# Optimization experiments

Measured on AMD Instinct MI355X. Metric: run time of the kernel, lower is better.

## Reference

```python
import jax, jax.numpy as jnp
import numpy as np

N_NODES = 50000


def gin_conv(x, src, dst, W, b, eps=0.0):
    # GINConv: nn((1+eps)*x_i + sum_{j in N(i)} x_j)
    agg = jax.ops.segment_sum(x[src], dst, num_segments=N_NODES)  # [N, D]
    h = (1.0 + eps) * x + agg
    return h @ W + b


def setup_inputs() -> dict:
    key = jax.random.key(0)
    ks = jax.random.split(key, 8)
    n, e = N_NODES, 800000
    d_in, d_h, d_out = 128, 128, 64
    feature = jax.random.normal(ks[0], (n, d_in), dtype=jnp.float32)
    edge_index = jax.random.randint(ks[1], (2, e), 0, n, dtype=jnp.int64)
    s1 = 1.0 / np.sqrt(d_in)
    sh = 1.0 / np.sqrt(d_h)
    W1 = jax.random.normal(ks[2], (d_in, d_h), dtype=jnp.float32) * s1
    b1 = jnp.zeros((d_h,), dtype=jnp.float32)
    Wh = jax.random.normal(ks[3], (d_h, d_h), dtype=jnp.float32) * sh
    bh = jnp.zeros((d_h,), dtype=jnp.float32)
    Wo = jax.random.normal(ks[4], (d_h, d_out), dtype=jnp.float32) * sh
    bo = jnp.zeros((d_out,), dtype=jnp.float32)
    return {"feature": feature, "edge_index": edge_index, "W1": W1, "b1": b1,
            "Wh": Wh, "bh": bh, "Wo": Wo, "bo": bo}


def reference(feature, edge_index, W1, b1, Wh, bh, Wo, bo):
    src, dst = edge_index[0], edge_index[1]
    x = gin_conv(feature, src, dst, W1, b1)
    x = jax.nn.relu(x)
    # one hidden layer (layer_num=3); dropout disabled (eval)
    x = gin_conv(x, src, dst, Wh, bh)
    x = jax.nn.relu(x)
    x = gin_conv(x, src, dst, Wo, bo)
    return jax.nn.log_softmax(x, axis=1)
```

## Files before the change

### kernel.cpp

```cpp
#include <hip/hip_runtime.h>

typedef short short8 __attribute__((ext_vector_type(8)));
typedef float f32x4 __attribute__((ext_vector_type(4)));


__device__ inline unsigned short f2bf(float f) {
    union { float f; unsigned u; } v; v.f = f;
    unsigned r = v.u + 0x7fffu + ((v.u >> 16) & 1u);
    return (unsigned short)(r >> 16);
}
__device__ inline unsigned pack2(float a, float b) {
    return (unsigned)f2bf(a) | ((unsigned)f2bf(b) << 16);
}
__device__ inline float bflo(unsigned u) { union { unsigned q; float f; } c; c.q = u << 16; return c.f; }
__device__ inline float bfhi(unsigned u) { union { unsigned q; float f; } c; c.q = u & 0xffff0000u; return c.f; }

#define ACC8(vv)                                     \
    acc[0] += bflo(vv.x); acc[1] += bfhi(vv.x);      \
    acc[2] += bflo(vv.y); acc[3] += bfhi(vv.y);      \
    acc[4] += bflo(vv.z); acc[5] += bfhi(vv.z);      \
    acc[6] += bflo(vv.w); acc[7] += bfhi(vv.w);

template <int TPN, typename F>
__device__ __forceinline__ void gather_acc(float acc[8], const uint4* __restrict__ x,
                                           int lane, int beg, int end, F geti) {
    int k = beg;
    for (; k + 8 <= end; k += 8) {
        int idx[8];
#pragma unroll
        for (int j = 0; j < 8; j++) idx[j] = geti(k + j);
        uint4 v[8];
#pragma unroll
        for (int j = 0; j < 8; j++) v[j] = x[(size_t)idx[j] * TPN + lane];
#pragma unroll
        for (int j = 0; j < 8; j++) { ACC8(v[j]) }
    }
    for (; k + 4 <= end; k += 4) {
        int i0 = geti(k), i1 = geti(k + 1), i2 = geti(k + 2), i3 = geti(k + 3);
        uint4 v0 = x[(size_t)i0 * TPN + lane];
        uint4 v1 = x[(size_t)i1 * TPN + lane];
        uint4 v2 = x[(size_t)i2 * TPN + lane];
        uint4 v3 = x[(size_t)i3 * TPN + lane];
        ACC8(v0) ACC8(v1) ACC8(v2) ACC8(v3)
    }
    for (; k < end; ++k) {
        uint4 v0 = x[(size_t)geti(k) * TPN + lane];
        ACC8(v0)
    }
}


#define EPB 2048
#define NE 8
#define BSH 9
#define MAXBKT 128
#define DCAP 10240
#define BCAP 16384

__global__ __launch_bounds__(256) void megaA(
    const int* __restrict__ src, const int* __restrict__ dst,
    int* __restrict__ cursor, unsigned* __restrict__ pairs,
    int e, int nbkt, int nblk,
    const float4* __restrict__ feat, uint2* __restrict__ featb, int cvtb, int nf4,
    const float* __restrict__ W1, const float* __restrict__ Wh, const float* __restrict__ Wo,
    unsigned short* __restrict__ W1t, unsigned short* __restrict__ Wht,
    unsigned short* __restrict__ Wot) {
    __shared__ int hist[MAXBKT], loff[MAXBKT], cur[MAXBKT], gb[MAXBKT];
    __shared__ int sc[256];
    __shared__ unsigned sorted[EPB];
    int t = threadIdx.x, blk = blockIdx.x;
    if (blk < nblk) {
        for (int b = t; b < nbkt; b += 256) hist[b] = 0;
        __syncthreads();
        int base = blk * EPB;
        int cnt = min(EPB, e - base);
        unsigned packed[NE];
        int bb[NE];
#pragma unroll
        for (int j = 0; j < NE; j++) {
            int idx = base + t + 256 * j;
            bb[j] = -1;
            if (idx < e) {
                unsigned s0 = (unsigned)src[idx], d = (unsigned)dst[idx];
                int b = (int)(d >> BSH);
                bb[j] = b;
                packed[j] = s0 | ((d & ((1u << BSH) - 1)) << 16) | ((unsigned)b << 25);
                atomicAdd(&hist[b], 1);
            }
        }
        __syncthreads();
        int v = (t < nbkt) ? hist[t] : 0;
        sc[t] = v;
        __syncthreads();
        for (int off = 1; off < 256; off <<= 1) {
            int u = (t >= off) ? sc[t - off] : 0;
            __syncthreads();
            sc[t] += u;
            __syncthreads();
        }
        if (t < nbkt) {
            int ex = sc[t] - v;
            loff[t] = ex;
            cur[t] = ex;
            gb[t] = t * BCAP + (v ? atomicAdd(&cursor[t], v) : atomicAdd(&cursor[t], 0));
        }
        __syncthreads();
#pragma unroll
        for (int j = 0; j < NE; j++) {
            if (bb[j] >= 0) {
                int r = atomicAdd(&cur[bb[j]], 1);
                sorted[r] = packed[j];
            }
        }
        __syncthreads();
        for (int i = t; i < cnt; i += 256) {
            unsigned w = sorted[i];
            int b = (int)(w >> 25);
            pairs[gb[b] + (i - loff[b])] = w;
        }
    } else if (blk < nblk + cvtb) {
        int i = (blk - nblk) * 256 + t;
        if (i < nf4) {
            float4 v = feat[i];
            featb[i] = make_uint2(pack2(v.x, v.y), pack2(v.z, v.w));
        }
    } else {
        int i = (blk - nblk - cvtb) * 256 + t;
        if (i < 16384) {
            int k = i >> 7, nn = i & 127;
            W1t[nn * 128 + k] = f2bf(W1[i]);
        } else if (i < 32768) {
            int j = i - 16384, k = j >> 7, nn = j & 127;
            Wht[nn * 128 + k] = f2bf(Wh[j]);
        } else if (i < 40960) {
            int j = i - 32768, k = j >> 6, nn = j & 63;
            Wot[nn * 128 + k] = f2bf(Wo[j]);
        }
    }
}

__global__ __launch_bounds__(512) void buildD(const unsigned* __restrict__ pairs,
                                              const int* __restrict__ cursor,
                                              int* __restrict__ row_ptr, int* __restrict__ row_end,
                                              unsigned short* __restrict__ csr, int n) {
    __shared__ int hist[512], off[512];
    __shared__ unsigned short lcsr[DCAP];
    int t = threadIdx.x, b = blockIdx.x;
    int cnt = cursor[b], base = b * BCAP;
    hist[t] = 0;
    __syncthreads();
    for (int i = t; i < cnt; i += 512)
        atomicAdd(&hist[(pairs[base + i] >> 16) & 511], 1);
    __syncthreads();
    int v = hist[t];
    off[t] = v;
    __syncthreads();
    for (int o = 1; o < 512; o <<= 1) {
        int u = (t >= o) ? off[t - o] : 0;
        __syncthreads();
        off[t] += u;
        __syncthreads();
    }
    int excl = off[t] - v;
    int node = (b << BSH) + t;
    if (node < n) {
        row_ptr[node] = base + excl;
        row_end[node] = base + off[t];
    }
    __syncthreads();
    hist[t] = excl;
    __syncthreads();
    for (int i = t; i < cnt; i += 512) {
        unsigned w = pairs[base + i];
        int r = atomicAdd(&hist[(w >> 16) & 511], 1);
        if (r < DCAP) lcsr[r] = (unsigned short)(w & 0xFFFFu);
    }
    __syncthreads();
    int lim = min(cnt, DCAP);
    for (int i = t; i < lim; i += 512) csr[base + i] = lcsr[i];
}


#define ECAP 1024

template <bool SECOND>
__global__ __launch_bounds__(256) void fused_layer(
    const uint4* __restrict__ x, const int* __restrict__ row_ptr,
    const int* __restrict__ row_end, const unsigned short* __restrict__ csr,
    const short8* __restrict__ Bt, const float* __restrict__ bias,
    unsigned short* __restrict__ out_h,
    const short8* __restrict__ Bt2,
    unsigned short* __restrict__ out_y,
    int n) {
    __shared__ unsigned short As[16][136];
    __shared__ unsigned short Hs[SECOND ? 16 : 1][SECOND ? 136 : 1];
    __shared__ unsigned short eidx[ECAP];

    int t = threadIdx.x;
    int nl = t >> 4, chunk = t & 15;
    int r0 = blockIdx.x * 16;
    int node = r0 + nl;

    int E0 = row_ptr[min(r0, n - 1)];
    int E1 = row_end[min(r0 + 15, n - 1)];
    int ecnt = min(E1 - E0, ECAP);
    for (int i = t; i < ecnt; i += 256) eidx[i] = csr[E0 + i];
    __syncthreads();

    float acc[8] = {0.f, 0.f, 0.f, 0.f, 0.f, 0.f, 0.f, 0.f};
    if (node < n) {
        uint4 s0 = x[(size_t)node * 16 + chunk];
        ACC8(s0)
        int beg = row_ptr[node], end = row_end[node];
        if (E1 - E0 <= ECAP) {
            gather_acc<16>(acc, x, chunk, beg - E0, end - E0,
                           [&](int k) { return (int)eidx[k]; });
        } else {
            gather_acc<16>(acc, x, chunk, beg, end,
                           [&](int k) { return (int)csr[k]; });
        }
    }
    uint4 packed;
    packed.x = pack2(acc[0], acc[1]); packed.y = pack2(acc[2], acc[3]);
    packed.z = pack2(acc[4], acc[5]); packed.w = pack2(acc[6], acc[7]);
    ((uint4*)&As[nl][0])[chunk] = packed;
    __syncthreads();

    int wid = t >> 6, lane = t & 63;
    int lm = lane & 15, lq = lane >> 4;

    short8 a[4];
#pragma unroll
    for (int kc = 0; kc < 4; kc++)
        a[kc] = *(const short8*)&As[lm][kc * 32 + lq * 8];

    f32x4 hacc[2];
#pragma unroll
    for (int nt = 0; nt < 2; nt++) hacc[nt] = (f32x4){0.f, 0.f, 0.f, 0.f};
#pragma unroll
    for (int nt = 0; nt < 2; nt++) {
        const short8* Br = Bt + (size_t)((wid * 2 + nt) * 16 + lm) * 16;
#pragma unroll
        for (int kc = 0; kc < 4; kc++)
            hacc[nt] = __builtin_amdgcn_mfma_f32_16x16x32_bf16(a[kc], Br[kc * 4 + lq], hacc[nt], 0, 0, 0);
    }

#pragma unroll
    for (int nt = 0; nt < 2; nt++) {
        int col = (wid * 2 + nt) * 16 + lm;
        float bv = bias[col];
#pragma unroll
        for (int i = 0; i < 4; i++) {
            int row = r0 + lq * 4 + i;
            float v = fmaxf(hacc[nt][i] + bv, 0.f);
            if (SECOND) {
                Hs[lq * 4 + i][col] = f2bf(v);
            } else if (row < n) {
                out_h[(size_t)row * 128 + col] = f2bf(v);
            }
        }
    }

    if (SECOND) {
        __syncthreads();
        short8 a2[4];
#pragma unroll
        for (int kc = 0; kc < 4; kc++)
            a2[kc] = *(const short8*)&Hs[lm][kc * 32 + lq * 8];
        f32x4 yacc = (f32x4){0.f, 0.f, 0.f, 0.f};
        const short8* Br2 = Bt2 + (size_t)(wid * 16 + lm) * 16;
#pragma unroll
        for (int kc = 0; kc < 4; kc++)
            yacc = __builtin_amdgcn_mfma_f32_16x16x32_bf16(a2[kc], Br2[kc * 4 + lq], yacc, 0, 0, 0);
        int col = wid * 16 + lm;
#pragma unroll
        for (int i = 0; i < 4; i++) {
            int row = r0 + lq * 4 + i;
            if (row < n) out_y[(size_t)row * 64 + col] = f2bf(yacc[i]);
        }
    }
}


#define ECAP2 1536

__global__ __launch_bounds__(256) void agg_lsm(
    const uint4* __restrict__ x, float* __restrict__ out,
    const int* __restrict__ row_ptr, const int* __restrict__ row_end,
    const unsigned short* __restrict__ csr, const float* __restrict__ bo, int n) {
    __shared__ unsigned short eidx[ECAP2];
    int t = threadIdx.x;
    int r0 = blockIdx.x * 32;
    int node = r0 + (t >> 3), lane = t & 7;

    int E0 = row_ptr[min(r0, n - 1)];
    int E1 = row_end[min(r0 + 31, n - 1)];
    int ecnt = min(E1 - E0, ECAP2);
    for (int i = t; i < ecnt; i += 256) eidx[i] = csr[E0 + i];
    __syncthreads();

    if (node >= n) return;
    uint4 s0 = x[(size_t)node * 8 + lane];
    float acc[8] = { bflo(s0.x), bfhi(s0.x), bflo(s0.y), bfhi(s0.y),
                     bflo(s0.z), bfhi(s0.z), bflo(s0.w), bfhi(s0.w) };
    int beg = row_ptr[node], end = row_end[node];
    if (E1 - E0 <= ECAP2) {
        gather_acc<8>(acc, x, lane, beg - E0, end - E0,
                      [&](int k) { return (int)eidx[k]; });
    } else {
        gather_acc<8>(acc, x, lane, beg, end,
                      [&](int k) { return (int)csr[k]; });
    }

    const float4* bo4 = (const float4*)bo;
    float4 bA = bo4[lane * 2], bB = bo4[lane * 2 + 1];
    acc[0] += bA.x; acc[1] += bA.y; acc[2] += bA.z; acc[3] += bA.w;
    acc[4] += bB.x; acc[5] += bB.y; acc[6] += bB.z; acc[7] += bB.w;
    float m = acc[0];
#pragma unroll
    for (int j = 1; j < 8; j++) m = fmaxf(m, acc[j]);
#pragma unroll
    for (int off = 1; off < 8; off <<= 1) m = fmaxf(m, __shfl_xor(m, off, 64));
    float s = 0.f;
#pragma unroll
    for (int j = 0; j < 8; j++) s += __expf(acc[j] - m);
#pragma unroll
    for (int off = 1; off < 8; off <<= 1) s += __shfl_xor(s, off, 64);
    float ls = m + __logf(s);
    float4 o0 = make_float4(acc[0] - ls, acc[1] - ls, acc[2] - ls, acc[3] - ls);
    float4 o1 = make_float4(acc[4] - ls, acc[5] - ls, acc[6] - ls, acc[7] - ls);
    float4* op = (float4*)(out + (size_t)node * 64 + lane * 8);
    op[0] = o0;
    op[1] = o1;
}


extern "C" void kernel_launch(void* const* d_in, const int* in_sizes, int n_in,
                              void* d_out, int out_size, void* d_ws, size_t ws_size,
                              hipStream_t stream) {
    const float* feature = (const float*)d_in[0];
    const int*   edges   = (const int*)d_in[1];
    const float* W1 = (const float*)d_in[2];
    const float* b1 = (const float*)d_in[3];
    const float* Wh = (const float*)d_in[4];
    const float* bh = (const float*)d_in[5];
    const float* Wo = (const float*)d_in[6];
    const float* bo = (const float*)d_in[7];

    int n = in_sizes[0] / 128;
    int e = in_sizes[1] / 2;
    const int* src = edges;
    const int* dst = edges + e;

    int nbkt = (n + 511) >> BSH;
    int nblk = (e + EPB - 1) / EPB;
    int nf4 = n * 32;
    int cvtb = (nf4 + 255) / 256;

    char* ws = (char*)d_ws;
    auto take = [&](size_t bytes) {
        char* p = ws;
        ws += (bytes + 255) & ~(size_t)255;
        return p;
    };
    int* cursor  = (int*)take((size_t)nbkt * 4);
    int* row_ptr = (int*)take((size_t)n * 4);
    int* row_end = (int*)take((size_t)n * 4);
    unsigned* pairs = (unsigned*)take((size_t)nbkt * BCAP * 4);
    unsigned short* csr = (unsigned short*)take((size_t)nbkt * BCAP * 2);
    unsigned short* featb = (unsigned short*)take((size_t)n * 128 * 2);
    unsigned short* hb    = (unsigned short*)take((size_t)n * 128 * 2);
    unsigned short* yb    = (unsigned short*)take((size_t)n * 64 * 2);
    unsigned short* W1t = (unsigned short*)take(128 * 128 * 2);
    unsigned short* Wht = (unsigned short*)take(128 * 128 * 2);
    unsigned short* Wot = (unsigned short*)take(64 * 128 * 2);

    hipMemsetAsync(cursor, 0, (size_t)nbkt * 4, stream);
    megaA<<<nblk + cvtb + 160, 256, 0, stream>>>(
        src, dst, cursor, pairs, e, nbkt, nblk,
        (const float4*)feature, (uint2*)featb, cvtb, nf4,
        W1, Wh, Wo, W1t, Wht, Wot);
    buildD<<<nbkt, 512, 0, stream>>>(pairs, cursor, row_ptr, row_end, csr, n);

    int fblocks = (n + 15) / 16;

    fused_layer<false><<<fblocks, 256, 0, stream>>>(
        (const uint4*)featb, row_ptr, row_end, csr, (const short8*)W1t, b1,
        hb, nullptr, nullptr, n);

    fused_layer<true><<<fblocks, 256, 0, stream>>>(
        (const uint4*)hb, row_ptr, row_end, csr, (const short8*)Wht, bh,
        nullptr, (const short8*)Wot, yb, n);

    agg_lsm<<<(n + 31) / 32, 256, 0, stream>>>(
        (const uint4*)yb, (float*)d_out, row_ptr, row_end, csr, bo, n);
}
```

Measured before the change: 209.6 us.

## Split each node's edge gather across lane groups with shuffle reduction

The gather/aggregate loops in the fused layer and final aggregation kernels are restructured so that each wavefront handles a few nodes at a time, with lane groups working on interleaved edges of the same node. Partial sums are then combined through cross-lane xor shuffles. The goal is to reduce load imbalance from uneven node degrees and to expose more independent memory loads per node. In exchange it adds shuffle reductions, a serial loop over nodes per wave, and an extra shared-memory staging buffer in the final kernel. It also changes the fp32 summation order.

Result: slower. 229.6 us (+9.5%).

```diff
diff --git a/kernel.cpp b/kernel.cpp
--- a/kernel.cpp
+++ b/kernel.cpp
@@ -21,31 +21,21 @@
     acc[4] += bflo(vv.z); acc[5] += bfhi(vv.z);      \
     acc[6] += bflo(vv.w); acc[7] += bfhi(vv.w);
 
-template <int TPN, typename F>
-__device__ __forceinline__ void gather_acc(float acc[8], const uint4* __restrict__ x,
-                                           int lane, int beg, int end, F geti) {
-    int k = beg;
-    for (; k + 8 <= end; k += 8) {
-        int idx[8];
-#pragma unroll
-        for (int j = 0; j < 8; j++) idx[j] = geti(k + j);
-        uint4 v[8];
-#pragma unroll
-        for (int j = 0; j < 8; j++) v[j] = x[(size_t)idx[j] * TPN + lane];
-#pragma unroll
-        for (int j = 0; j < 8; j++) { ACC8(v[j]) }
-    }
-    for (; k + 4 <= end; k += 4) {
-        int i0 = geti(k), i1 = geti(k + 1), i2 = geti(k + 2), i3 = geti(k + 3);
-        uint4 v0 = x[(size_t)i0 * TPN + lane];
-        uint4 v1 = x[(size_t)i1 * TPN + lane];
-        uint4 v2 = x[(size_t)i2 * TPN + lane];
-        uint4 v3 = x[(size_t)i3 * TPN + lane];
+template <int TPN, int EW, typename F>
+__device__ __forceinline__ void node_gather(float acc[8], const uint4* __restrict__ x,
+                                            int chunk, int eo, int beg, int end, F geti) {
+    int k = beg + eo;
+    for (; k + 3 * EW < end; k += 4 * EW) {
+        int i0 = geti(k), i1 = geti(k + EW), i2 = geti(k + 2 * EW), i3 = geti(k + 3 * EW);
+        uint4 v0 = x[(size_t)i0 * TPN + chunk];
+        uint4 v1 = x[(size_t)i1 * TPN + chunk];
+        uint4 v2 = x[(size_t)i2 * TPN + chunk];
+        uint4 v3 = x[(size_t)i3 * TPN + chunk];
         ACC8(v0) ACC8(v1) ACC8(v2) ACC8(v3)
     }
-    for (; k < end; ++k) {
-        uint4 v0 = x[(size_t)geti(k) * TPN + lane];
-        ACC8(v0)
+    for (; k < end; k += EW) {
+        uint4 v = x[(size_t)geti(k) * TPN + chunk];
+        ACC8(v)
     }
 }
 
@@ -197,36 +187,50 @@
     __shared__ unsigned short eidx[ECAP];
 
     int t = threadIdx.x;
-    int nl = t >> 4, chunk = t & 15;
     int r0 = blockIdx.x * 16;
-    int node = r0 + nl;
+    int wid = t >> 6, lane = t & 63;
+    int chunk = lane & 15, eo = lane >> 4;
 
     int E0 = row_ptr[min(r0, n - 1)];
     int E1 = row_end[min(r0 + 15, n - 1)];
     int ecnt = min(E1 - E0, ECAP);
+    bool staged = (E1 - E0) <= ECAP;
     for (int i = t; i < ecnt; i += 256) eidx[i] = csr[E0 + i];
     __syncthreads();
 
-    float acc[8] = {0.f, 0.f, 0.f, 0.f, 0.f, 0.f, 0.f, 0.f};
-    if (node < n) {
-        uint4 s0 = x[(size_t)node * 16 + chunk];
-        ACC8(s0)
-        int beg = row_ptr[node], end = row_end[node];
-        if (E1 - E0 <= ECAP) {
-            gather_acc<16>(acc, x, chunk, beg - E0, end - E0,
-                           [&](int k) { return (int)eidx[k]; });
-        } else {
-            gather_acc<16>(acc, x, chunk, beg, end,
-                           [&](int k) { return (int)csr[k]; });
-        }
-    }
-    uint4 packed;
-    packed.x = pack2(acc[0], acc[1]); packed.y = pack2(acc[2], acc[3]);
-    packed.z = pack2(acc[4], acc[5]); packed.w = pack2(acc[6], acc[7]);
-    ((uint4*)&As[nl][0])[chunk] = packed;
-    __syncthreads();
-
-    int wid = t >> 6, lane = t & 63;
+#pragma unroll
+    for (int nd = 0; nd < 4; nd++) {
+        int nl = wid * 4 + nd;
+        int node = r0 + nl;
+        float acc[8] = {0.f, 0.f, 0.f, 0.f, 0.f, 0.f, 0.f, 0.f};
+        if (node < n) {
+            if (eo == 0) {
+                uint4 s0 = x[(size_t)node * 16 + chunk];
+                ACC8(s0)
+            }
+            int beg = row_ptr[node], end = row_end[node];
+            if (staged) {
+                node_gather<16, 4>(acc, x, chunk, eo, beg - E0, end - E0,
+                                   [&](int k) { return (int)eidx[k]; });
+            } else {
+                node_gather<16, 4>(acc, x, chunk, eo, beg, end,
+                                   [&](int k) { return (int)csr[k]; });
+            }
+        }
+#pragma unroll
+        for (int j = 0; j < 8; j++) {
+            acc[j] += __shfl_xor(acc[j], 16, 64);
+            acc[j] += __shfl_xor(acc[j], 32, 64);
+        }
+        if (eo == 0) {
+            uint4 packed;
+            packed.x = pack2(acc[0], acc[1]); packed.y = pack2(acc[2], acc[3]);
+            packed.z = pack2(acc[4], acc[5]); packed.w = pack2(acc[6], acc[7]);
+            ((uint4*)&As[nl][0])[chunk] = packed;
+        }
+    }
+    __syncthreads();
+
     int lm = lane & 15, lq = lane >> 4;
 
     short8 a[4];
@@ -289,31 +293,59 @@
     const int* __restrict__ row_ptr, const int* __restrict__ row_end,
     const unsigned short* __restrict__ csr, const float* __restrict__ bo, int n) {
     __shared__ unsigned short eidx[ECAP2];
+    __shared__ float Zs[32][72];
     int t = threadIdx.x;
     int r0 = blockIdx.x * 32;
-    int node = r0 + (t >> 3), lane = t & 7;
+    int wid = t >> 6, lane = t & 63;
+    int chunk = lane & 7, eo = lane >> 3;
 
     int E0 = row_ptr[min(r0, n - 1)];
     int E1 = row_end[min(r0 + 31, n - 1)];
     int ecnt = min(E1 - E0, ECAP2);
+    bool staged = (E1 - E0) <= ECAP2;
     for (int i = t; i < ecnt; i += 256) eidx[i] = csr[E0 + i];
     __syncthreads();
 
+#pragma unroll
+    for (int nd = 0; nd < 8; nd++) {
+        int nl = wid * 8 + nd;
+        int node = r0 + nl;
+        float acc[8] = {0.f, 0.f, 0.f, 0.f, 0.f, 0.f, 0.f, 0.f};
+        if (node < n) {
+            if (eo == 0) {
+                uint4 s0 = x[(size_t)node * 8 + chunk];
+                ACC8(s0)
+            }
+            int beg = row_ptr[node], end = row_end[node];
+            if (staged) {
+                node_gather<8, 8>(acc, x, chunk, eo, beg - E0, end - E0,
+                                  [&](int k) { return (int)eidx[k]; });
+            } else {
+                node_gather<8, 8>(acc, x, chunk, eo, beg, end,
+                                  [&](int k) { return (int)csr[k]; });
+            }
+        }
+#pragma unroll
+        for (int j = 0; j < 8; j++) {
+            acc[j] += __shfl_xor(acc[j], 8, 64);
+            acc[j] += __shfl_xor(acc[j], 16, 64);
+            acc[j] += __shfl_xor(acc[j], 32, 64);
+        }
+        if (eo == 0) {
+#pragma unroll
+            for (int j = 0; j < 8; j++) Zs[nl][chunk * 8 + j] = acc[j];
+        }
+    }
+    __syncthreads();
+
+    int nl = t >> 3, col = t & 7;
+    int node = r0 + nl;
     if (node >= n) return;
-    uint4 s0 = x[(size_t)node * 8 + lane];
-    float acc[8] = { bflo(s0.x), bfhi(s0.x), bflo(s0.y), bfhi(s0.y),
-                     bflo(s0.z), bfhi(s0.z), bflo(s0.w), bfhi(s0.w) };
-    int beg = row_ptr[node], end = row_end[node];
-    if (E1 - E0 <= ECAP2) {
-        gather_acc<8>(acc, x, lane, beg - E0, end - E0,
-                      [&](int k) { return (int)eidx[k]; });
-    } else {
-        gather_acc<8>(acc, x, lane, beg, end,
-                      [&](int k) { return (int)csr[k]; });
-    }
-
+    float acc[8];
+#pragma unroll
+    for (int j = 0; j < 8; j++) acc[j] = Zs[nl][col * 8 + j];
     const float4* bo4 = (const float4*)bo;
-    float4 bA = bo4[lane * 2], bB = bo4[lane * 2 + 1];
+    float4 bA = bo4[col * 2], bB = bo4[col * 2 + 1];
     acc[0] += bA.x; acc[1] += bA.y; acc[2] += bA.z; acc[3] += bA.w;
     acc[4] += bB.x; acc[5] += bB.y; acc[6] += bB.z; acc[7] += bB.w;
     float m = acc[0];
@@ -329,7 +361,7 @@
     float ls = m + __logf(s);
     float4 o0 = make_float4(acc[0] - ls, acc[1] - ls, acc[2] - ls, acc[3] - ls);
     float4 o1 = make_float4(acc[4] - ls, acc[5] - ls, acc[6] - ls, acc[7] - ls);
-    float4* op = (float4*)(out + (size_t)node * 64 + lane * 8);
+    float4* op = (float4*)(out + (size_t)node * 64 + col * 8);
     op[0] = o0;
     op[1] = o1;
 }
```

## Split aggregation and GEMM into separate kernels with column-plane feature layout

Applied to the files above, without the earlier changes.

Features are now stored in 32-column planes, and aggregation runs per plane with four edge slots per node combined by shuffles. This is meant to shrink the gather working set per block so it stays in cache and to raise parallelism. The dense transforms become standalone MFMA GEMM kernels, and the final log-softmax gets its own kernel reading an fp32 intermediate. The cost is extra launches plus writing and re-reading the aggregated and fp32 intermediates through global memory, where the fused version kept them in shared memory.

After: 257.3 us. 1.23x slower.

```diff
diff --git a/kernel.cpp b/kernel.cpp
--- a/kernel.cpp
+++ b/kernel.cpp
@@ -2,6 +2,7 @@
 
 typedef short short8 __attribute__((ext_vector_type(8)));
 typedef float f32x4 __attribute__((ext_vector_type(4)));
+typedef unsigned u32x4 __attribute__((ext_vector_type(4)));
 
 
 __device__ inline unsigned short f2bf(float f) {
@@ -20,34 +21,6 @@
     acc[2] += bflo(vv.y); acc[3] += bfhi(vv.y);      \
     acc[4] += bflo(vv.z); acc[5] += bfhi(vv.z);      \
     acc[6] += bflo(vv.w); acc[7] += bfhi(vv.w);
-
-template <int TPN, typename F>
-__device__ __forceinline__ void gather_acc(float acc[8], const uint4* __restrict__ x,
-                                           int lane, int beg, int end, F geti) {
-    int k = beg;
-    for (; k + 8 <= end; k += 8) {
-        int idx[8];
-#pragma unroll
-        for (int j = 0; j < 8; j++) idx[j] = geti(k + j);
-        uint4 v[8];
-#pragma unroll
-        for (int j = 0; j < 8; j++) v[j] = x[(size_t)idx[j] * TPN + lane];
-#pragma unroll
-        for (int j = 0; j < 8; j++) { ACC8(v[j]) }
-    }
-    for (; k + 4 <= end; k += 4) {
-        int i0 = geti(k), i1 = geti(k + 1), i2 = geti(k + 2), i3 = geti(k + 3);
-        uint4 v0 = x[(size_t)i0 * TPN + lane];
-        uint4 v1 = x[(size_t)i1 * TPN + lane];
-        uint4 v2 = x[(size_t)i2 * TPN + lane];
-        uint4 v3 = x[(size_t)i3 * TPN + lane];
-        ACC8(v0) ACC8(v1) ACC8(v2) ACC8(v3)
-    }
-    for (; k < end; ++k) {
-        uint4 v0 = x[(size_t)geti(k) * TPN + lane];
-        ACC8(v0)
-    }
-}
 
 
 #define EPB 2048
@@ -61,7 +34,7 @@
     const int* __restrict__ src, const int* __restrict__ dst,
     int* __restrict__ cursor, unsigned* __restrict__ pairs,
     int e, int nbkt, int nblk,
-    const float4* __restrict__ feat, uint2* __restrict__ featb, int cvtb, int nf4,
+    const float4* __restrict__ feat, uint4* __restrict__ featb, int cvtb, int n16, int np,
     const float* __restrict__ W1, const float* __restrict__ Wh, const float* __restrict__ Wo,
     unsigned short* __restrict__ W1t, unsigned short* __restrict__ Wht,
     unsigned short* __restrict__ Wot) {
@@ -120,9 +93,13 @@
         }
     } else if (blk < nblk + cvtb) {
         int i = (blk - nblk) * 256 + t;
-        if (i < nf4) {
-            float4 v = feat[i];
-            featb[i] = make_uint2(pack2(v.x, v.y), pack2(v.z, v.w));
+        if (i < n16) {
+            int node = i >> 4, chunk = i & 15;
+            int q = chunk >> 2, c4 = chunk & 3;
+            float4 a = feat[2 * i], b = feat[2 * i + 1];
+            uint4 pk = make_uint4(pack2(a.x, a.y), pack2(a.z, a.w),
+                                  pack2(b.x, b.y), pack2(b.z, b.w));
+            featb[(size_t)q * (np * 4) + (size_t)node * 4 + c4] = pk;
         }
     } else {
         int i = (blk - nblk - cvtb) * 256 + t;
@@ -183,139 +160,178 @@
 
 #define ECAP 1024
 
-template <bool SECOND>
-__global__ __launch_bounds__(256) void fused_layer(
-    const uint4* __restrict__ x, const int* __restrict__ row_ptr,
-    const int* __restrict__ row_end, const unsigned short* __restrict__ csr,
-    const short8* __restrict__ Bt, const float* __restrict__ bias,
-    unsigned short* __restrict__ out_h,
-    const short8* __restrict__ Bt2,
-    unsigned short* __restrict__ out_y,
-    int n) {
-    __shared__ unsigned short As[16][136];
-    __shared__ unsigned short Hs[SECOND ? 16 : 1][SECOND ? 136 : 1];
+template <int NSPLIT, bool OUTF32>
+__global__ __launch_bounds__(256) void agg_plane(
+    const uint4* __restrict__ x, void* __restrict__ outp,
+    const int* __restrict__ row_ptr, const int* __restrict__ row_end,
+    const unsigned short* __restrict__ csr, int n, int np) {
     __shared__ unsigned short eidx[ECAP];
-
+    int q = (int)(blockIdx.x % NSPLIT);
+    int nb = (int)(blockIdx.x / NSPLIT);
     int t = threadIdx.x;
-    int nl = t >> 4, chunk = t & 15;
-    int r0 = blockIdx.x * 16;
+    int r0 = nb * 16;
+    int wid = t >> 6, lane = t & 63;
+    int group = lane >> 4;
+    int chunk4 = lane & 3;
+    int eslot = (lane >> 2) & 3;
+    int nl = wid * 4 + group;
     int node = r0 + nl;
 
     int E0 = row_ptr[min(r0, n - 1)];
     int E1 = row_end[min(r0 + 15, n - 1)];
     int ecnt = min(E1 - E0, ECAP);
-    for (int i = t; i < ecnt; i += 256) eidx[i] = csr[E0 + i];
-    __syncthreads();
-
+    bool staged = (E1 - E0) <= ECAP;
+    for (int i = t; i < ecnt; i += 256)
+        eidx[i] = __builtin_nontemporal_load(&csr[E0 + i]);
+    __syncthreads();
+
+    const uint4* xq = x + (size_t)q * np * 4;
     float acc[8] = {0.f, 0.f, 0.f, 0.f, 0.f, 0.f, 0.f, 0.f};
     if (node < n) {
-        uint4 s0 = x[(size_t)node * 16 + chunk];
-        ACC8(s0)
+        if (eslot == 0) {
+            uint4 s0 = xq[(size_t)node * 4 + chunk4];
+            ACC8(s0)
+        }
         int beg = row_ptr[node], end = row_end[node];
-        if (E1 - E0 <= ECAP) {
-            gather_acc<16>(acc, x, chunk, beg - E0, end - E0,
-                           [&](int k) { return (int)eidx[k]; });
+        if (staged) {
+            beg -= E0; end -= E0;
+            int k = beg + eslot;
+            for (; k + 12 < end; k += 16) {
+                int i0 = eidx[k], i1 = eidx[k + 4], i2 = eidx[k + 8], i3 = eidx[k + 12];
+                uint4 v0 = xq[(size_t)i0 * 4 + chunk4];
+                uint4 v1 = xq[(size_t)i1 * 4 + chunk4];
+                uint4 v2 = xq[(size_t)i2 * 4 + chunk4];
+                uint4 v3 = xq[(size_t)i3 * 4 + chunk4];
+                ACC8(v0) ACC8(v1) ACC8(v2) ACC8(v3)
+            }
+            for (; k < end; k += 4) {
+                uint4 v = xq[(size_t)eidx[k] * 4 + chunk4];
+                ACC8(v)
+            }
         } else {
-            gather_acc<16>(acc, x, chunk, beg, end,
-                           [&](int k) { return (int)csr[k]; });
-        }
-    }
-    uint4 packed;
-    packed.x = pack2(acc[0], acc[1]); packed.y = pack2(acc[2], acc[3]);
-    packed.z = pack2(acc[4], acc[5]); packed.w = pack2(acc[6], acc[7]);
-    ((uint4*)&As[nl][0])[chunk] = packed;
-    __syncthreads();
-
-    int wid = t >> 6, lane = t & 63;
-    int lm = lane & 15, lq = lane >> 4;
-
+            int k = beg + eslot;
+            for (; k + 12 < end; k += 16) {
+                int i0 = csr[k], i1 = csr[k + 4], i2 = csr[k + 8], i3 = csr[k + 12];
+                uint4 v0 = xq[(size_t)i0 * 4 + chunk4];
+                uint4 v1 = xq[(size_t)i1 * 4 + chunk4];
+                uint4 v2 = xq[(size_t)i2 * 4 + chunk4];
+                uint4 v3 = xq[(size_t)i3 * 4 + chunk4];
+                ACC8(v0) ACC8(v1) ACC8(v2) ACC8(v3)
+            }
+            for (; k < end; k += 4) {
+                uint4 v = xq[(size_t)csr[k] * 4 + chunk4];
+                ACC8(v)
+            }
+        }
+    }
+#pragma unroll
+    for (int j = 0; j < 8; j++) {
+        acc[j] += __shfl_xor(acc[j], 4, 64);
+        acc[j] += __shfl_xor(acc[j], 8, 64);
+    }
+    if (node < n && eslot == 0) {
+        if (OUTF32) {
+            f32x4* o = (f32x4*)((float*)outp + (size_t)node * 64 + (q * 4 + chunk4) * 8);
+            f32x4 o0 = {acc[0], acc[1], acc[2], acc[3]};
+            f32x4 o1 = {acc[4], acc[5], acc[6], acc[7]};
+            __builtin_nontemporal_store(o0, o);
+            __builtin_nontemporal_store(o1, o + 1);
+        } else {
+            u32x4 pk = {pack2(acc[0], acc[1]), pack2(acc[2], acc[3]),
+                        pack2(acc[4], acc[5]), pack2(acc[6], acc[7])};
+            __builtin_nontemporal_store(
+                pk, (u32x4*)outp + (size_t)q * np * 4 + (size_t)node * 4 + chunk4);
+        }
+    }
+}
+
+
+template <int OUT, bool SECOND>
+__global__ __launch_bounds__(256) void gemm_mfma(
+    const short8* __restrict__ A,
+    const short8* __restrict__ Bt,
+    const float* __restrict__ bias, unsigned short* __restrict__ outp,
+    const short8* __restrict__ Bt2, unsigned short* __restrict__ out_y,
+    int n, int np) {
+    constexpr int NT = OUT / 16;
+    __shared__ unsigned short Hs[SECOND ? 4 : 1][16][136];
+    int t = threadIdx.x;
+    int wid = t >> 6, lane = t & 63, lm = lane & 15, lq = lane >> 4;
+    int r0 = blockIdx.x * 64 + wid * 16;
+    int arow = min(r0 + lm, n - 1);
     short8 a[4];
 #pragma unroll
     for (int kc = 0; kc < 4; kc++)
-        a[kc] = *(const short8*)&As[lm][kc * 32 + lq * 8];
-
-    f32x4 hacc[2];
-#pragma unroll
-    for (int nt = 0; nt < 2; nt++) hacc[nt] = (f32x4){0.f, 0.f, 0.f, 0.f};
-#pragma unroll
-    for (int nt = 0; nt < 2; nt++) {
-        const short8* Br = Bt + (size_t)((wid * 2 + nt) * 16 + lm) * 16;
+        a[kc] = A[((size_t)kc * np + arow) * 4 + lq];
+
+    f32x4 acc[NT];
+#pragma unroll
+    for (int nt = 0; nt < NT; nt++) acc[nt] = (f32x4){0.f, 0.f, 0.f, 0.f};
+#pragma unroll
+    for (int nt = 0; nt < NT; nt++) {
+        const short8* Br = Bt + (size_t)(nt * 16 + lm) * 16;
 #pragma unroll
         for (int kc = 0; kc < 4; kc++)
-            hacc[nt] = __builtin_amdgcn_mfma_f32_16x16x32_bf16(a[kc], Br[kc * 4 + lq], hacc[nt], 0, 0, 0);
-    }
-
-#pragma unroll
-    for (int nt = 0; nt < 2; nt++) {
-        int col = (wid * 2 + nt) * 16 + lm;
+            acc[nt] = __builtin_amdgcn_mfma_f32_16x16x32_bf16(a[kc], Br[kc * 4 + lq], acc[nt], 0, 0, 0);
+    }
+
+#pragma unroll
+    for (int nt = 0; nt < NT; nt++) {
+        int col = nt * 16 + lm;
         float bv = bias[col];
 #pragma unroll
         for (int i = 0; i < 4; i++) {
             int row = r0 + lq * 4 + i;
-            float v = fmaxf(hacc[nt][i] + bv, 0.f);
+            float v = fmaxf(acc[nt][i] + bv, 0.f);
             if (SECOND) {
-                Hs[lq * 4 + i][col] = f2bf(v);
+                Hs[wid][lq * 4 + i][col] = f2bf(v);
             } else if (row < n) {
-                out_h[(size_t)row * 128 + col] = f2bf(v);
+                outp[((size_t)(col >> 5) * np + row) * 32 + (col & 31)] = f2bf(v);
             }
         }
     }
 
     if (SECOND) {
-        __syncthreads();
         short8 a2[4];
 #pragma unroll
         for (int kc = 0; kc < 4; kc++)
-            a2[kc] = *(const short8*)&Hs[lm][kc * 32 + lq * 8];
-        f32x4 yacc = (f32x4){0.f, 0.f, 0.f, 0.f};
-        const short8* Br2 = Bt2 + (size_t)(wid * 16 + lm) * 16;
-#pragma unroll
-        for (int kc = 0; kc < 4; kc++)
-            yacc = __builtin_amdgcn_mfma_f32_16x16x32_bf16(a2[kc], Br2[kc * 4 + lq], yacc, 0, 0, 0);
-        int col = wid * 16 + lm;
-#pragma unroll
-        for (int i = 0; i < 4; i++) {
-            int row = r0 + lq * 4 + i;
-            if (row < n) out_y[(size_t)row * 64 + col] = f2bf(yacc[i]);
-        }
-    }
-}
-
-
-#define ECAP2 1536
-
-__global__ __launch_bounds__(256) void agg_lsm(
-    const uint4* __restrict__ x, float* __restrict__ out,
-    const int* __restrict__ row_ptr, const int* __restrict__ row_end,
-    const unsigned short* __restrict__ csr, const float* __restrict__ bo, int n) {
-    __shared__ unsigned short eidx[ECAP2];
+            a2[kc] = *(const short8*)&Hs[wid][lm][kc * 32 + lq * 8];
+        f32x4 yacc[4];
+#pragma unroll
+        for (int ct = 0; ct < 4; ct++) yacc[ct] = (f32x4){0.f, 0.f, 0.f, 0.f};
+#pragma unroll
+        for (int ct = 0; ct < 4; ct++) {
+            const short8* Br2 = Bt2 + (size_t)(ct * 16 + lm) * 16;
+#pragma unroll
+            for (int kc = 0; kc < 4; kc++)
+                yacc[ct] = __builtin_amdgcn_mfma_f32_16x16x32_bf16(a2[kc], Br2[kc * 4 + lq], yacc[ct], 0, 0, 0);
+        }
+#pragma unroll
+        for (int ct = 0; ct < 4; ct++) {
+            int col = ct * 16 + lm;
+#pragma unroll
+            for (int i = 0; i < 4; i++) {
+                int row = r0 + lq * 4 + i;
+                if (row < n)
+                    out_y[((size_t)(col >> 5) * np + row) * 32 + (col & 31)] = f2bf(yacc[ct][i]);
+            }
+        }
+    }
+}
+
+
+__global__ __launch_bounds__(256) void lsm_kernel(const float4* __restrict__ z,
+                                                  const float* __restrict__ bo,
+                                                  float* __restrict__ out, int n) {
     int t = threadIdx.x;
-    int r0 = blockIdx.x * 32;
-    int node = r0 + (t >> 3), lane = t & 7;
-
-    int E0 = row_ptr[min(r0, n - 1)];
-    int E1 = row_end[min(r0 + 31, n - 1)];
-    int ecnt = min(E1 - E0, ECAP2);
-    for (int i = t; i < ecnt; i += 256) eidx[i] = csr[E0 + i];
-    __syncthreads();
-
+    int node = blockIdx.x * 32 + (t >> 3), lane = t & 7;
     if (node >= n) return;
-    uint4 s0 = x[(size_t)node * 8 + lane];
-    float acc[8] = { bflo(s0.x), bfhi(s0.x), bflo(s0.y), bfhi(s0.y),
-                     bflo(s0.z), bfhi(s0.z), bflo(s0.w), bfhi(s0.w) };
-    int beg = row_ptr[node], end = row_end[node];
-    if (E1 - E0 <= ECAP2) {
-        gather_acc<8>(acc, x, lane, beg - E0, end - E0,
-                      [&](int k) { return (int)eidx[k]; });
-    } else {
-        gather_acc<8>(acc, x, lane, beg, end,
-                      [&](int k) { return (int)csr[k]; });
-    }
-
+    float4 v0 = z[(size_t)node * 16 + lane * 2];
+    float4 v1 = z[(size_t)node * 16 + lane * 2 + 1];
     const float4* bo4 = (const float4*)bo;
     float4 bA = bo4[lane * 2], bB = bo4[lane * 2 + 1];
-    acc[0] += bA.x; acc[1] += bA.y; acc[2] += bA.z; acc[3] += bA.w;
-    acc[4] += bB.x; acc[5] += bB.y; acc[6] += bB.z; acc[7] += bB.w;
+    float acc[8] = { v0.x + bA.x, v0.y + bA.y, v0.z + bA.z, v0.w + bA.w,
+                     v1.x + bB.x, v1.y + bB.y, v1.z + bB.z, v1.w + bB.w };
     float m = acc[0];
 #pragma unroll
     for (int j = 1; j < 8; j++) m = fmaxf(m, acc[j]);
@@ -327,11 +343,9 @@
 #pragma unroll
     for (int off = 1; off < 8; off <<= 1) s += __shfl_xor(s, off, 64);
     float ls = m + __logf(s);
-    float4 o0 = make_float4(acc[0] - ls, acc[1] - ls, acc[2] - ls, acc[3] - ls);
-    float4 o1 = make_float4(acc[4] - ls, acc[5] - ls, acc[6] - ls, acc[7] - ls);
     float4* op = (float4*)(out + (size_t)node * 64 + lane * 8);
-    op[0] = o0;
-    op[1] = o1;
+    op[0] = make_float4(acc[0] - ls, acc[1] - ls, acc[2] - ls, acc[3] - ls);
+    op[1] = make_float4(acc[4] - ls, acc[5] - ls, acc[6] - ls, acc[7] - ls);
 }
 
 
@@ -351,11 +365,12 @@
     int e = in_sizes[1] / 2;
     const int* src = edges;
     const int* dst = edges + e;
+    int np = n;
 
     int nbkt = (n + 511) >> BSH;
     int nblk = (e + EPB - 1) / EPB;
-    int nf4 = n * 32;
-    int cvtb = (nf4 + 255) / 256;
+    int n16 = n * 16;
+    int cvtb = (n16 + 255) / 256;
 
     char* ws = (char*)d_ws;
     auto take = [&](size_t bytes) {
@@ -369,8 +384,10 @@
     unsigned* pairs = (unsigned*)take((size_t)nbkt * BCAP * 4);
     unsigned short* csr = (unsigned short*)take((size_t)nbkt * BCAP * 2);
     unsigned short* featb = (unsigned short*)take((size_t)n * 128 * 2);
+    unsigned short* aggb  = (unsigned short*)take((size_t)n * 128 * 2);
     unsigned short* hb    = (unsigned short*)take((size_t)n * 128 * 2);
     unsigned short* yb    = (unsigned short*)take((size_t)n * 64 * 2);
+    float*          zf    = (float*)take((size_t)n * 64 * 4);
     unsigned short* W1t = (unsigned short*)take(128 * 128 * 2);
     unsigned short* Wht = (unsigned short*)take(128 * 128 * 2);
     unsigned short* Wot = (unsigned short*)take(64 * 128 * 2);
@@ -378,20 +395,24 @@
     hipMemsetAsync(cursor, 0, (size_t)nbkt * 4, stream);
     megaA<<<nblk + cvtb + 160, 256, 0, stream>>>(
         src, dst, cursor, pairs, e, nbkt, nblk,
-        (const float4*)feature, (uint2*)featb, cvtb, nf4,
+        (const float4*)feature, (uint4*)featb, cvtb, n16, np,
         W1, Wh, Wo, W1t, Wht, Wot);
     buildD<<<nbkt, 512, 0, stream>>>(pairs, cursor, row_ptr, row_end, csr, n);
 
     int fblocks = (n + 15) / 16;
 
-    fused_layer<false><<<fblocks, 256, 0, stream>>>(
-        (const uint4*)featb, row_ptr, row_end, csr, (const short8*)W1t, b1,
-        hb, nullptr, nullptr, n);
-
-    fused_layer<true><<<fblocks, 256, 0, stream>>>(
-        (const uint4*)hb, row_ptr, row_end, csr, (const short8*)Wht, bh,
-        nullptr, (const short8*)Wot, yb, n);
-
-    agg_lsm<<<(n + 31) / 32, 256, 0, stream>>>(
-        (const uint4*)yb, (float*)d_out, row_ptr, row_end, csr, bo, n);
-}
+    agg_plane<4, false><<<fblocks * 4, 256, 0, stream>>>(
+        (const uint4*)featb, aggb, row_ptr, row_end, csr, n, np);
+    gemm_mfma<128, false><<<(n + 63) / 64, 256, 0, stream>>>(
+        (const short8*)aggb, (const short8*)W1t, b1, hb, nullptr, nullptr, n, np);
+
+    agg_plane<4, false><<<fblocks * 4, 256, 0, stream>>>(
+        (const uint4*)hb, aggb, row_ptr, row_end, csr, n, np);
+    gemm_mfma<128, true><<<(n + 63) / 64, 256, 0, stream>>>(
+        (const short8*)aggb, (const short8*)Wht, bh, nullptr, (const short8*)Wot, yb, n, np);
+
+    agg_plane<2, true><<<fblocks * 2, 256, 0, stream>>>(
+        (const uint4*)yb, zf, row_ptr, row_end, csr, n, np);
+    lsm_kernel<<<(n + 31) / 32, 256, 0, stream>>>(
+        (const float4*)zf, bo, (float*)d_out, n);
+}
```
